# Kernel tuning notes

Measured on AMD Instinct MI355X. Metric: run time of the kernel, lower is better.

The kernel has to match this reference:

```python
import jax, jax.numpy as jnp
import numpy as np

W_RESIDUAL = 0.5  # cfg.MODEL.TRM.RESIDUAL weight
EPS = 1e-12      # F.normalize eps


def _l2norm(x, axis):
    n = jnp.sqrt(jnp.sum(x * x, axis=axis, keepdims=True))
    return x / jnp.maximum(n, EPS)


def setup_inputs() -> dict:
    key = jax.random.key(0)
    k1, k2, k3, k4 = jax.random.split(key, 4)
    B, NS, NP, C, T = 32, 16, 8, 256, 128
    return {
        "map2d_iou": jax.random.normal(k1, (B, C, T, T), dtype=jnp.float32),
        "sent_feat": jax.random.normal(k2, (B, NS, C), dtype=jnp.float32),
        "phrase_feat": jax.random.normal(k3, (B, NS, NP, C), dtype=jnp.float32),
        "phrase_weight": jax.random.uniform(k4, (B, NS, NP), dtype=jnp.float32),
        "phrase_mask": jnp.ones((B, NS, NP), dtype=jnp.float32),
    }


def reference(map2d_iou, sent_feat, phrase_feat, phrase_weight, phrase_mask):
    B, C, T, _ = map2d_iou.shape
    NS, NP = phrase_feat.shape[1], phrase_feat.shape[2]
    # valid 2D proposals: start <= end (upper triangular)
    mask2d = jnp.triu(jnp.ones((T, T), dtype=map2d_iou.dtype))

    # F.normalize(vid_feat_iou, dim=0) per video, flattened to (B, C, T*T)
    vid_norm = _l2norm(map2d_iou, axis=1).reshape(B, C, T * T)

    # phrase scores: normalize each phrase feat over C, mm with video map
    ph_norm = _l2norm(phrase_feat, axis=-1)                       # B,NS,NP,C
    ph_scores = jnp.einsum("bspc,bcm->bspm", ph_norm, vid_norm)   # B,NS,NP,T*T
    phrase_score_map = (jax.nn.sigmoid(ph_scores * 10.0).reshape(B, NS, NP, T, T)
                        * mask2d * phrase_mask[:, :, :, None, None])

    # phrase-weighted aggregation: (B,NS,1,NP) @ (B,NS,NP,T*T)
    ph_att = jnp.einsum("bsp,bspm->bsm", phrase_weight, ph_scores).reshape(B, NS, T, T)

    # sentence scores
    sf_norm = _l2norm(sent_feat, axis=-1)                         # B,NS,C
    sf_scores = jnp.einsum("bsc,bcm->bsm", sf_norm, vid_norm).reshape(B, NS, T, T)

    iou_scores = jax.nn.sigmoid((sf_scores + W_RESIDUAL * ph_att) * 10.0) * mask2d
    return iou_scores, phrase_score_map
```

## Files before the change

kernel.cpp:

```cpp
#include <hip/hip_runtime.h>
#include <hip/hip_bf16.h>

#define B_   32
#define NS_  16
#define NP_  8
#define C_   256
#define T_   128
#define M_   (T_*T_)
#define NF_  144
#define MT_  128
#define KC_  32
#define NCH_ (C_/KC_)

typedef __attribute__((ext_vector_type(4))) float f32x4;
typedef __attribute__((ext_vector_type(8))) short s16x8;
typedef __attribute__((ext_vector_type(4))) short s16x4;
typedef __attribute__((ext_vector_type(4))) int   i32x4;
typedef __attribute__((ext_vector_type(2))) int   i32x2;

#define KSTR 20
#define SUBT 644
#define VBUF 5152
#define ABUF_DW 2304

#define LDS_BYTES 39040
#define AB_OFF    20608

__device__ __forceinline__ short f2bf(float f) {
  unsigned u = __builtin_bit_cast(unsigned, f);
  u += 0x7fffu + ((u >> 16) & 1u);
  return (short)(u >> 16);
}
__device__ __forceinline__ int cvt_pk_bf16(float a, float b) {
  int d;
  asm("v_cvt_pk_bf16_f32 %0, %1, %2" : "=v"(d) : "v"(a), "v"(b));
  return d;
}
__device__ __forceinline__ float sigm(float z) { return 1.0f / (1.0f + __expf(-z)); }

__global__ void prep_feats(const float* __restrict__ sf, const float* __restrict__ pf,
                           short* __restrict__ Fb) {
  const int bs = blockIdx.x;
  const int b  = bs >> 4, s = bs & 15;
  const int t  = threadIdx.x;
  __shared__ float red[4];
  const int kc   = t >> 5;
  const int kk   = t & 31;
  const int half = kk >> 4;
  const int g    = (kk & 15) >> 2;
  const int j    = kk & 3;
  const int pos  = 8 * g + 4 * half + j;
  for (int v = 0; v < 9; ++v) {
    float x = (v < 8) ? pf[(((size_t)bs) * NP_ + v) * C_ + t]
                      : sf[((size_t)bs) * C_ + t];
    float ss = x * x;
    #pragma unroll
    for (int off = 32; off; off >>= 1) ss += __shfl_xor(ss, off);
    __syncthreads();
    if ((t & 63) == 0) red[t >> 6] = ss;
    __syncthreads();
    const float tot = red[0] + red[1] + red[2] + red[3];
    const float rn = 1.0f / fmaxf(sqrtf(tot), 1e-12f);
    const int row = (v < 8) ? (s * NP_ + v) : (128 + s);
    Fb[(((size_t)(b * 8 + kc)) * NF_ + row) * 32 + pos] = f2bf(x * rn);
  }
}

__global__ void __launch_bounds__(256, 4) trm_main(
    const float* __restrict__ V,
    const int* __restrict__ FbD,
    const float* __restrict__ pw,
    const float* __restrict__ pm,
    float* __restrict__ out0,
    float* __restrict__ out1) {
  __shared__ __align__(16) char smem[LDS_BYTES];
  short* vb  = (short*)smem;
  int*   abI = (int*)(smem + AB_OFF);
  short* abS = (short*)(smem + AB_OFF);
  float* pbuf = (float*)(smem + AB_OFF);
  float* rnl  = (float*)(smem + AB_OFF + 4096);
  float* att  = (float*)(smem + AB_OFF + 4608);
  float* pwl  = (float*)(smem + AB_OFF + 13056);
  float* pml  = (float*)(smem + AB_OFF + 13568);

  const int tid  = threadIdx.x;
  const int b    = blockIdx.y;
  const int tile = blockIdx.x;
  const int m0   = tile * MT_;

  const int c4 = tid & 31;
  const int q  = tid >> 5;
  const size_t vbase = ((size_t)b * C_) * M_ + m0 + c4 * 4;
  const int smt  = c4 >> 2;
  const int scc0 = (c4 & 3) * 4;

  const int lane = tid & 63;
  const int w  = tid >> 6;
  const int g  = lane >> 4;
  const int cc = lane & 15;

  f32x4 acc[9][2];
  #pragma unroll
  for (int i = 0; i < 9; ++i) {
    #pragma unroll
    for (int n = 0; n < 2; ++n) acc[i][n] = (f32x4){0.f, 0.f, 0.f, 0.f};
  }

  float4 r[4];
  i32x4 a0, a1;
  int a2;
  float ssq0 = 0.f, ssq1 = 0.f, ssq2 = 0.f, ssq3 = 0.f;

  const int* AbBase = FbD + (size_t)b * 8 * ABUF_DW;

  #pragma unroll
  for (int i = 0; i < 4; ++i) r[i] = *(const float4*)(V + vbase + (size_t)(q + i * 8) * M_);
  {
    const int* Ab = AbBase;
    a0 = *(const i32x4*)(Ab + tid * 4);
    a1 = *(const i32x4*)(Ab + 1024 + tid * 4);
    a2 = Ab[2048 + tid];
  }
  #pragma unroll
  for (int i = 0; i < 4; ++i) {
    const int kk = q + i * 8;
    ssq0 += r[i].x * r[i].x; ssq1 += r[i].y * r[i].y;
    ssq2 += r[i].z * r[i].z; ssq3 += r[i].w * r[i].w;
    i32x2 pk = {cvt_pk_bf16(r[i].x, r[i].y), cvt_pk_bf16(r[i].z, r[i].w)};
    *(i32x2*)(&vb[smt * SUBT + kk * KSTR + scc0]) = pk;
  }
  {
    int* Ad = abI;
    *(i32x4*)(Ad + tid * 4) = a0;
    *(i32x4*)(Ad + 1024 + tid * 4) = a1;
    Ad[2048 + tid] = a2;
  }
  __syncthreads();

  int cur = 0;
  for (int kc = 0; kc < NCH_; ++kc) {
    if (kc < NCH_ - 1) {
      #pragma unroll
      for (int i = 0; i < 4; ++i)
        r[i] = *(const float4*)(V + vbase + (size_t)((kc + 1) * KC_ + q + i * 8) * M_);
      const int* Ab = AbBase + (kc + 1) * ABUF_DW;
      a0 = *(const i32x4*)(Ab + tid * 4);
      a1 = *(const i32x4*)(Ab + 1024 + tid * 4);
      a2 = Ab[2048 + tid];
    }
    {
      s16x8 bf[2];
      #pragma unroll
      for (int n = 0; n < 2; ++n) {
        const int mt = 2 * w + n;
        const int base = cur * VBUF + mt * SUBT + cc;
        #pragma unroll
        for (int j = 0; j < 4; ++j) {
          bf[n][j]     = vb[base + (4 * g + j) * KSTR];
          bf[n][j + 4] = vb[base + (16 + 4 * g + j) * KSTR];
        }
      }
      const short* Arow = abS + cur * (ABUF_DW * 2) + cc * 32 + g * 8;
      #pragma unroll
      for (int ft = 0; ft < 9; ++ft) {
        const s16x8 af = *(const s16x8*)(Arow + ft * (16 * 32));
        acc[ft][0] = __builtin_amdgcn_mfma_f32_16x16x32_bf16(af, bf[0], acc[ft][0], 0, 0, 0);
        acc[ft][1] = __builtin_amdgcn_mfma_f32_16x16x32_bf16(af, bf[1], acc[ft][1], 0, 0, 0);
      }
    }
    if (kc < NCH_ - 1) {
      #pragma unroll
      for (int i = 0; i < 4; ++i) {
        const int kk = q + i * 8;
        ssq0 += r[i].x * r[i].x; ssq1 += r[i].y * r[i].y;
        ssq2 += r[i].z * r[i].z; ssq3 += r[i].w * r[i].w;
        i32x2 pk = {cvt_pk_bf16(r[i].x, r[i].y), cvt_pk_bf16(r[i].z, r[i].w)};
        *(i32x2*)(&vb[(cur ^ 1) * VBUF + smt * SUBT + kk * KSTR + scc0]) = pk;
      }
      int* Ad = abI + (cur ^ 1) * ABUF_DW;
      *(i32x4*)(Ad + tid * 4) = a0;
      *(i32x4*)(Ad + 1024 + tid * 4) = a1;
      Ad[2048 + tid] = a2;
      __syncthreads();
      cur ^= 1;
    }
  }

  __syncthreads();

  {
    f32x4 p = {ssq0, ssq1, ssq2, ssq3};
    *(f32x4*)(&pbuf[q * 128 + c4 * 4]) = p;
  }
  if (tid < 128) { pwl[tid] = pw[b * 128 + tid]; pml[tid] = pm[b * 128 + tid]; }
  __syncthreads();
  if (tid < 128) {
    float ss = 0.f;
    #pragma unroll
    for (int qq = 0; qq < 8; ++qq) ss += pbuf[qq * 128 + tid];
    rnl[tid] = 1.0f / fmaxf(sqrtf(ss), 1e-12f);
  }
  __syncthreads();

  #pragma unroll
  for (int n = 0; n < 2; ++n) {
    const int col = (2 * w + n) * 16 + cc;
    const float rn = rnl[col];
    const int m = m0 + col;
    const float msk = (col >= tile) ? 1.0f : 0.0f;
    #pragma unroll
    for (int ft = 0; ft < 8; ++ft) {
      float pa = 0.f;
      #pragma unroll
      for (int rr = 0; rr < 4; ++rr) {
        const int f = ft * 16 + 4 * g + rr;
        const float raw = acc[ft][n][rr] * rn;
        out1[(((size_t)(b * NS_ + (f >> 3)) * NP_ + (f & 7)) << 14) + m] =
            sigm(10.0f * raw) * msk * pml[f];
        pa += pwl[f] * raw;
      }
      pa += __shfl_xor(pa, 16);
      if ((g & 1) == 0) att[(2 * ft + (g >> 1)) * 132 + col] = pa;
    }
  }
  __syncthreads();
  #pragma unroll
  for (int n = 0; n < 2; ++n) {
    const int col = (2 * w + n) * 16 + cc;
    const float rn = rnl[col];
    const int m = m0 + col;
    const float msk = (col >= tile) ? 1.0f : 0.0f;
    #pragma unroll
    for (int rr = 0; rr < 4; ++rr) {
      const int s = 4 * g + rr;
      const float sfv = acc[8][n][rr] * rn;
      const float pa = att[s * 132 + col];
      out0[(((size_t)(b * NS_ + s)) << 14) + m] = sigm(10.0f * (sfv + 0.5f * pa)) * msk;
    }
  }
}

extern "C" void kernel_launch(void* const* d_in, const int* in_sizes, int n_in,
                              void* d_out, int out_size, void* d_ws, size_t ws_size,
                              hipStream_t stream) {
  const float* V  = (const float*)d_in[0];
  const float* sf = (const float*)d_in[1];
  const float* pf = (const float*)d_in[2];
  const float* pw = (const float*)d_in[3];
  const float* pm = (const float*)d_in[4];
  float* out0 = (float*)d_out;
  float* out1 = out0 + (size_t)B_ * NS_ * M_;
  short* Fb = (short*)d_ws;

  prep_feats<<<B_ * NS_, 256, 0, stream>>>(sf, pf, Fb);
  dim3 grid(M_ / MT_, B_);
  trm_main<<<grid, 256, 0, stream>>>(V, (const int*)Fb, pw, pm, out0, out1);
}
```

Before: 253.9 us.

## Use direct global-to-LDS loads for features, deepen V prefetch, nontemporal stores

The feature tiles are now copied straight from global memory into LDS with global_load_lds, so they no longer pass through registers. The video-map loads are prefetched two chunks ahead using alternating register sets, with explicit vmcnt waits and barriers in place of __syncthreads. The main loop is fully unrolled, and output stores are marked nontemporal so they bypass cache retention. The aim is more overlap between HBM loads and MFMA work and fewer register round-trips. In exchange, register pressure is higher and the hand-written waitcnt logic is fragile.

```diff
diff --git a/kernel.cpp b/kernel.cpp
--- a/kernel.cpp
+++ b/kernel.cpp
@@ -14,13 +14,13 @@
 
 typedef __attribute__((ext_vector_type(4))) float f32x4;
 typedef __attribute__((ext_vector_type(8))) short s16x8;
-typedef __attribute__((ext_vector_type(4))) short s16x4;
 typedef __attribute__((ext_vector_type(4))) int   i32x4;
 typedef __attribute__((ext_vector_type(2))) int   i32x2;
 
 #define KSTR 20
 #define SUBT 644
 #define VBUF 5152
+#define ABUF_B  9216
 #define ABUF_DW 2304
 
 #define LDS_BYTES 39040
@@ -75,7 +75,6 @@
     float* __restrict__ out1) {
   __shared__ __align__(16) char smem[LDS_BYTES];
   short* vb  = (short*)smem;
-  int*   abI = (int*)(smem + AB_OFF);
   short* abS = (short*)(smem + AB_OFF);
   float* pbuf = (float*)(smem + AB_OFF);
   float* rnl  = (float*)(smem + AB_OFF + 4096);
@@ -106,83 +105,91 @@
     for (int n = 0; n < 2; ++n) acc[i][n] = (f32x4){0.f, 0.f, 0.f, 0.f};
   }
 
-  float4 r[4];
-  i32x4 a0, a1;
-  int a2;
+  float4 rA[4], rB[4];
   float ssq0 = 0.f, ssq1 = 0.f, ssq2 = 0.f, ssq3 = 0.f;
 
-  const int* AbBase = FbD + (size_t)b * 8 * ABUF_DW;
-
-  #pragma unroll
-  for (int i = 0; i < 4; ++i) r[i] = *(const float4*)(V + vbase + (size_t)(q + i * 8) * M_);
-  {
-    const int* Ab = AbBase;
-    a0 = *(const i32x4*)(Ab + tid * 4);
-    a1 = *(const i32x4*)(Ab + 1024 + tid * 4);
-    a2 = Ab[2048 + tid];
-  }
-  #pragma unroll
-  for (int i = 0; i < 4; ++i) {
-    const int kk = q + i * 8;
-    ssq0 += r[i].x * r[i].x; ssq1 += r[i].y * r[i].y;
-    ssq2 += r[i].z * r[i].z; ssq3 += r[i].w * r[i].w;
-    i32x2 pk = {cvt_pk_bf16(r[i].x, r[i].y), cvt_pk_bf16(r[i].z, r[i].w)};
-    *(i32x2*)(&vb[smt * SUBT + kk * KSTR + scc0]) = pk;
-  }
-  {
-    int* Ad = abI;
-    *(i32x4*)(Ad + tid * 4) = a0;
-    *(i32x4*)(Ad + 1024 + tid * 4) = a1;
-    Ad[2048 + tid] = a2;
-  }
-  __syncthreads();
-
-  int cur = 0;
+  const char* Ag = (const char*)FbD + (size_t)b * 8 * ABUF_B;
+
+  #define LOADA(kcn, bufn) do {                                                      \
+    const char* _s0 = Ag + (size_t)(kcn) * ABUF_B + w * 1024 + lane * 16;            \
+    char* _d0 = smem + AB_OFF + (bufn) * ABUF_B + w * 1024;                          \
+    __builtin_amdgcn_global_load_lds(                                                \
+        (const __attribute__((address_space(1))) void*)_s0,                          \
+        (__attribute__((address_space(3))) void*)_d0, 16, 0, 0);                     \
+    __builtin_amdgcn_global_load_lds(                                                \
+        (const __attribute__((address_space(1))) void*)(_s0 + 4096),                 \
+        (__attribute__((address_space(3))) void*)(_d0 + 4096), 16, 0, 0);            \
+    const char* _s2 = Ag + (size_t)(kcn) * ABUF_B + 8192 + w * 256 + lane * 4;       \
+    char* _d2 = smem + AB_OFF + (bufn) * ABUF_B + 8192 + w * 256;                    \
+    __builtin_amdgcn_global_load_lds(                                                \
+        (const __attribute__((address_space(1))) void*)_s2,                          \
+        (__attribute__((address_space(3))) void*)_d2, 4, 0, 0);                      \
+  } while (0)
+
+  #define FENCE() asm volatile("" ::: "memory")
+
+  #define LOADV(R, kcn) do {                                                         \
+    _Pragma("unroll")                                                                \
+    for (int _i = 0; _i < 4; ++_i)                                                   \
+      R[_i] = *(const float4*)(V + vbase + (size_t)((kcn) * KC_ + q + _i * 8) * M_); \
+  } while (0)
+
+  #define PACKV(R, bufn) do {                                                        \
+    _Pragma("unroll")                                                                \
+    for (int _i = 0; _i < 4; ++_i) {                                                 \
+      const int _kk = q + _i * 8;                                                    \
+      ssq0 += R[_i].x * R[_i].x; ssq1 += R[_i].y * R[_i].y;                          \
+      ssq2 += R[_i].z * R[_i].z; ssq3 += R[_i].w * R[_i].w;                          \
+      i32x2 _pk = {cvt_pk_bf16(R[_i].x, R[_i].y), cvt_pk_bf16(R[_i].z, R[_i].w)};    \
+      *(i32x2*)(&vb[(bufn) * VBUF + smt * SUBT + _kk * KSTR + scc0]) = _pk;          \
+    }                                                                                \
+  } while (0)
+
+  #define KBARN(n) do {                                                              \
+    asm volatile("s_waitcnt vmcnt(" #n ") lgkmcnt(0)" ::: "memory");                 \
+    __builtin_amdgcn_s_barrier();                                                    \
+    asm volatile("" ::: "memory");                                                   \
+  } while (0)
+
+  #define COMPUTE(bufn, kcn) do {                                                    \
+    s16x8 bf[2];                                                                     \
+    _Pragma("unroll")                                                                \
+    for (int _n = 0; _n < 2; ++_n) {                                                 \
+      const int _mt = 2 * w + _n;                                                    \
+      const int _base = (bufn) * VBUF + _mt * SUBT + cc;                             \
+      _Pragma("unroll")                                                              \
+      for (int _j = 0; _j < 4; ++_j) {                                               \
+        bf[_n][_j]     = vb[_base + (4 * g + _j) * KSTR];                            \
+        bf[_n][_j + 4] = vb[_base + (16 + 4 * g + _j) * KSTR];                       \
+      }                                                                              \
+    }                                                                                \
+    const short* _Arow = abS + (bufn) * (ABUF_DW * 2) + cc * 32 + g * 8;             \
+    _Pragma("unroll")                                                                \
+    for (int _ft = 0; _ft < 9; ++_ft) {                                              \
+      const s16x8 _af = *(const s16x8*)(_Arow + _ft * (16 * 32));                    \
+      acc[_ft][0] = __builtin_amdgcn_mfma_f32_16x16x32_bf16(_af, bf[0], acc[_ft][0], 0, 0, 0); \
+      acc[_ft][1] = __builtin_amdgcn_mfma_f32_16x16x32_bf16(_af, bf[1], acc[_ft][1], 0, 0, 0); \
+    }                                                                                \
+  } while (0)
+
+  LOADA(0, 0);
+  FENCE();
+  LOADV(rA, 0);
+  PACKV(rA, 0);
+  LOADV(rA, 1);
+  KBARN(4);
+
+  #pragma unroll
   for (int kc = 0; kc < NCH_; ++kc) {
+    if (kc < NCH_ - 1) { LOADA(kc + 1, (kc + 1) & 1); FENCE(); }
+    if (kc < NCH_ - 2) {
+      if (kc & 1) { LOADV(rA, kc + 2); } else { LOADV(rB, kc + 2); }
+      FENCE();
+    }
+    COMPUTE(kc & 1, kc);
     if (kc < NCH_ - 1) {
-      #pragma unroll
-      for (int i = 0; i < 4; ++i)
-        r[i] = *(const float4*)(V + vbase + (size_t)((kc + 1) * KC_ + q + i * 8) * M_);
-      const int* Ab = AbBase + (kc + 1) * ABUF_DW;
-      a0 = *(const i32x4*)(Ab + tid * 4);
-      a1 = *(const i32x4*)(Ab + 1024 + tid * 4);
-      a2 = Ab[2048 + tid];
-    }
-    {
-      s16x8 bf[2];
-      #pragma unroll
-      for (int n = 0; n < 2; ++n) {
-        const int mt = 2 * w + n;
-        const int base = cur * VBUF + mt * SUBT + cc;
-        #pragma unroll
-        for (int j = 0; j < 4; ++j) {
-          bf[n][j]     = vb[base + (4 * g + j) * KSTR];
-          bf[n][j + 4] = vb[base + (16 + 4 * g + j) * KSTR];
-        }
-      }
-      const short* Arow = abS + cur * (ABUF_DW * 2) + cc * 32 + g * 8;
-      #pragma unroll
-      for (int ft = 0; ft < 9; ++ft) {
-        const s16x8 af = *(const s16x8*)(Arow + ft * (16 * 32));
-        acc[ft][0] = __builtin_amdgcn_mfma_f32_16x16x32_bf16(af, bf[0], acc[ft][0], 0, 0, 0);
-        acc[ft][1] = __builtin_amdgcn_mfma_f32_16x16x32_bf16(af, bf[1], acc[ft][1], 0, 0, 0);
-      }
-    }
-    if (kc < NCH_ - 1) {
-      #pragma unroll
-      for (int i = 0; i < 4; ++i) {
-        const int kk = q + i * 8;
-        ssq0 += r[i].x * r[i].x; ssq1 += r[i].y * r[i].y;
-        ssq2 += r[i].z * r[i].z; ssq3 += r[i].w * r[i].w;
-        i32x2 pk = {cvt_pk_bf16(r[i].x, r[i].y), cvt_pk_bf16(r[i].z, r[i].w)};
-        *(i32x2*)(&vb[(cur ^ 1) * VBUF + smt * SUBT + kk * KSTR + scc0]) = pk;
-      }
-      int* Ad = abI + (cur ^ 1) * ABUF_DW;
-      *(i32x4*)(Ad + tid * 4) = a0;
-      *(i32x4*)(Ad + 1024 + tid * 4) = a1;
-      Ad[2048 + tid] = a2;
-      __syncthreads();
-      cur ^= 1;
+      if (kc & 1) { PACKV(rB, (kc + 1) & 1); } else { PACKV(rA, (kc + 1) & 1); }
+      if (kc < NCH_ - 2) { KBARN(4); } else { KBARN(0); }
     }
   }
 
@@ -215,8 +222,9 @@
       for (int rr = 0; rr < 4; ++rr) {
         const int f = ft * 16 + 4 * g + rr;
         const float raw = acc[ft][n][rr] * rn;
-        out1[(((size_t)(b * NS_ + (f >> 3)) * NP_ + (f & 7)) << 14) + m] =
-            sigm(10.0f * raw) * msk * pml[f];
+        __builtin_nontemporal_store(
+            sigm(10.0f * raw) * msk * pml[f],
+            &out1[(((size_t)(b * NS_ + (f >> 3)) * NP_ + (f & 7)) << 14) + m]);
         pa += pwl[f] * raw;
       }
       pa += __shfl_xor(pa, 16);
@@ -235,7 +243,9 @@
       const int s = 4 * g + rr;
       const float sfv = acc[8][n][rr] * rn;
       const float pa = att[s * 132 + col];
-      out0[(((size_t)(b * NS_ + s)) << 14) + m] = sigm(10.0f * (sfv + 0.5f * pa)) * msk;
+      __builtin_nontemporal_store(
+          sigm(10.0f * (sfv + 0.5f * pa)) * msk,
+          &out0[(((size_t)(b * NS_ + s)) << 14) + m]);
     }
   }
 }
```

Result: slower. 393.3 us (+54.9%).
